# Performance work log

Measured on AMD Instinct MI355X. Metric: run time of the kernel, lower is better.

Reference implementation:

```python
import jax, jax.numpy as jnp
import numpy as np

TEMP = 0.7
EPS = 1e-6
LN_EPS = 1e-5
CAP_FACTOR = 2.0


def setup_inputs() -> dict:
    key = jax.random.key(0)
    B, S, H, E = 8, 4096, 2048, 8
    H2 = H // 2
    ks = jax.random.split(key, 3)
    x = jax.random.normal(ks[0], (B, S, H), jnp.float32)
    ln_w = jnp.ones((H,), jnp.float32)
    ln_b = jnp.zeros((H,), jnp.float32)
    # kaiming_normal_(fan_in, relu): std = sqrt(2 / fan_in)
    w1 = jax.random.normal(ks[1], (H2, H), jnp.float32) * np.float32(np.sqrt(2.0 / H))
    b1 = jnp.zeros((H2,), jnp.float32)
    w2 = jax.random.normal(ks[2], (E, H2), jnp.float32) * np.float32(np.sqrt(2.0 / H2))
    b2 = jnp.zeros((E,), jnp.float32)
    return {"x": x, "ln_w": ln_w, "ln_b": ln_b, "w1": w1, "b1": b1,
            "w2": w2, "b2": b2, "top_k": 2, "num_experts": E}


def _forward(x, ln_w, ln_b, w1, b1, w2, b2, top_k, num_experts):
    B, S, H = x.shape
    N = B * S
    # router: LayerNorm -> Linear -> GELU(exact) -> Linear
    mu = x.mean(-1, keepdims=True)
    var = jnp.mean((x - mu) ** 2, axis=-1, keepdims=True)
    h = (x - mu) * jax.lax.rsqrt(var + LN_EPS) * ln_w + ln_b
    h = jax.nn.gelu(h @ w1.T + b1, approximate=False)
    logits = h @ w2.T + b2
    ew = jnp.clip(logits / TEMP, -50.0, 50.0)  # [B,S,E]

    flat = ew.reshape(N, num_experts)
    capacity = int(CAP_FACTOR * N * top_k / num_experts)

    # top-k per token + softmax over the k selected logits, scatter into dense mask
    tk_w, tk_i = jax.lax.top_k(flat, top_k)          # [N,k]
    sm = jax.nn.softmax(tk_w, axis=-1)               # [N,k]
    rows = jnp.arange(N)[:, None]
    masks = jnp.zeros((N, num_experts), flat.dtype).at[rows, tk_i].set(sm)

    # capacity drop: per expert column, if sum of weights > capacity keep only
    # the top-`capacity` weighted tokens (extra zero-valued picks are no-ops,
    # matching the torch min(capacity, nnz) behavior).
    cols = masks.T                                   # [E,N]
    sums = cols.sum(-1)                              # [E]
    kcap = min(capacity, N)
    tv, ti = jax.lax.top_k(cols, kcap)               # [E,kcap]
    erow = jnp.arange(num_experts)[:, None]
    capped = jnp.zeros_like(cols).at[erow, ti].set(tv)
    over = sums > capacity
    cols = jnp.where(over[:, None], capped, cols)
    count = jax.lax.stop_gradient(jnp.where(over, capped.sum(-1), sums))  # buffer, no grad

    masks = cols.T
    masks = masks / jnp.maximum(masks.sum(-1, keepdims=True), EPS)

    usage = count / jnp.maximum(count.sum(), EPS)
    target = jnp.full((num_experts,), 1.0 / num_experts, usage.dtype)
    # F.kl_div(log(usage), target, reduction='batchmean') with batch dim = E
    kl = jnp.sum(target * (jnp.log(target) - jnp.log(jnp.maximum(usage, EPS)))) / num_experts
    loss = 0.01 * kl
    return ew, masks.reshape(B, S, num_experts), loss, usage


def reference(x, ln_w, ln_b, w1, b1, w2, b2, top_k, num_experts):
    return _forward(x, ln_w, ln_b, w1, b1, w2, b2, top_k, num_experts)
```

## Files before the change

### kernel.cpp

```cpp
#include <hip/hip_runtime.h>
#include <math.h>

#define NTOK 32768
#define HDIM 2048
#define H2DIM 1024
#define NE 8

#define WS_MU 0
#define WS_RS 32768
#define WS_LOGITS 65536
#define WS_SUMS (65536 + 262144)
#define WS_W1_BYTES 1310976ull
#define WS_NEED (WS_W1_BYTES + 8388608ull)

#define OUT_MASKS 262144
#define OUT_LOSS 524288
#define OUT_USAGE 524289

typedef _Float16 half8 __attribute__((ext_vector_type(8)));
typedef float floatx16 __attribute__((ext_vector_type(16)));

#define H_SCALE 0.03125f
#define X_SCALE (0.03125f / 4096.0f)

__global__ __launch_bounds__(256) void w1prep_kernel(const float* __restrict__ w1,
                                                     _Float16* __restrict__ w1p) {
  int idx = blockIdx.x * 256 + threadIdx.x;
  int n = idx >> 6, kc = idx & 63;
  const float4* src = (const float4*)(w1 + (size_t)n * HDIM + kc * 32);
  float wv[32];
#pragma unroll
  for (int v = 0; v < 8; ++v) {
    float4 f = src[v];
    wv[v * 4 + 0] = f.x; wv[v * 4 + 1] = f.y;
    wv[v * 4 + 2] = f.z; wv[v * 4 + 3] = f.w;
  }
  _Float16 hi[32], lo[32];
#pragma unroll
  for (int v = 0; v < 32; ++v) {
    float t = wv[v] * 32.0f;
    hi[v] = (_Float16)t;
    lo[v] = (_Float16)((t - (float)hi[v]) * 4096.0f);
  }
  _Float16* dst = w1p + (size_t)idx * 64;
#pragma unroll
  for (int c = 0; c < 4; ++c) {
    half8 h = {hi[c*8+0],hi[c*8+1],hi[c*8+2],hi[c*8+3],hi[c*8+4],hi[c*8+5],hi[c*8+6],hi[c*8+7]};
    half8 l = {lo[c*8+0],lo[c*8+1],lo[c*8+2],lo[c*8+3],lo[c*8+4],lo[c*8+5],lo[c*8+6],lo[c*8+7]};
    *(half8*)&dst[c * 8] = h;
    *(half8*)&dst[32 + c * 8] = l;
  }
}

__global__ __launch_bounds__(256) void ln_stats_kernel(const float* __restrict__ x,
                                                       float* __restrict__ ws) {
  int g = blockIdx.x * 256 + threadIdx.x;
  if (g < NTOK * NE + NE) ws[WS_LOGITS + g] = 0.0f;

  int row = blockIdx.x * 4 + (threadIdx.x >> 6);
  int lane = threadIdx.x & 63;
  const float4* p = (const float4*)(x + (size_t)row * HDIM);
  float s = 0.f, sq = 0.f;
#pragma unroll
  for (int i = 0; i < 8; ++i) {
    float4 v = p[lane + 64 * i];
    s += (v.x + v.y) + (v.z + v.w);
    sq += (v.x * v.x + v.y * v.y) + (v.z * v.z + v.w * v.w);
  }
#pragma unroll
  for (int o = 32; o > 0; o >>= 1) {
    s += __shfl_xor(s, o);
    sq += __shfl_xor(sq, o);
  }
  if (lane == 0) {
    float m = s * (1.0f / HDIM);
    float var = fmaxf(sq * (1.0f / HDIM) - m * m, 0.0f);
    ws[WS_MU + row] = m;
    ws[WS_RS + row] = 1.0f / sqrtf(var + 1e-5f);
  }
}

#define LDB 40

__global__ __launch_bounds__(256, 2) void gemm_mfma_kernel(
    const float* __restrict__ x, const float* __restrict__ ln_w,
    const float* __restrict__ ln_b, const _Float16* __restrict__ w1p,
    const float* __restrict__ bias1, const float* __restrict__ w2,
    const float* __restrict__ mu, const float* __restrict__ rs,
    float* __restrict__ logits) {
  __shared__ _Float16 Ah[128 * LDB];
  __shared__ _Float16 Al[128 * LDB];
  __shared__ _Float16 Bh[128 * LDB];
  __shared__ _Float16 Bl[128 * LDB];

  const int tid = threadIdx.x;
  const int lin = blockIdx.x;
  const int xcd = lin & 7;
  const int jj = lin >> 3;
  const int m0 = (xcd * 32 + (jj >> 3)) * 128;
  const int n0 = (jj & 7) * 128;

  const int lane = tid & 63;
  const int wid = tid >> 6;
  const int wm = wid >> 1, wn = wid & 1;
  const int fr = lane & 31, fq = lane >> 5;

  const int am = tid >> 1, ak = (tid & 1) * 16;
  const float* xrow = x + (size_t)(m0 + am) * HDIM;
  const float ars = rs[m0 + am];
  const float amrs = -mu[m0 + am] * ars;
  const int bn = tid >> 1, bp = tid & 1;
  const _Float16* bsrc0 = w1p + (size_t)(n0 + bn) * 4096 + bp * 32;
  _Float16* bdst = (bp ? Bl : Bh) + bn * LDB;

  floatx16 acc_hh[2][2], acc_x[2][2];
#pragma unroll
  for (int i = 0; i < 2; ++i)
#pragma unroll
    for (int j = 0; j < 2; ++j)
#pragma unroll
      for (int r = 0; r < 16; ++r) { acc_hh[i][j][r] = 0.f; acc_x[i][j][r] = 0.f; }

  for (int kc = 0; kc < 64; ++kc) {
    const int k0 = kc * 32;
    const float4* xp = (const float4*)(xrow + k0 + ak);
    float4 xv0 = xp[0], xv1 = xp[1], xv2 = xp[2], xv3 = xp[3];
    const float4* lwp = (const float4*)(ln_w + k0 + ak);
    float4 lw0 = lwp[0], lw1 = lwp[1], lw2 = lwp[2], lw3 = lwp[3];
    const float4* lbp = (const float4*)(ln_b + k0 + ak);
    float4 lb0 = lbp[0], lb1 = lbp[1], lb2 = lbp[2], lb3 = lbp[3];
    const float4* bs = (const float4*)(bsrc0 + (size_t)kc * 64);
    float4 bv0 = bs[0], bv1 = bs[1], bv2 = bs[2], bv3 = bs[3];

    float xa[16] = {xv0.x,xv0.y,xv0.z,xv0.w, xv1.x,xv1.y,xv1.z,xv1.w,
                    xv2.x,xv2.y,xv2.z,xv2.w, xv3.x,xv3.y,xv3.z,xv3.w};
    float lwa[16] = {lw0.x,lw0.y,lw0.z,lw0.w, lw1.x,lw1.y,lw1.z,lw1.w,
                     lw2.x,lw2.y,lw2.z,lw2.w, lw3.x,lw3.y,lw3.z,lw3.w};
    float lba[16] = {lb0.x,lb0.y,lb0.z,lb0.w, lb1.x,lb1.y,lb1.z,lb1.w,
                     lb2.x,lb2.y,lb2.z,lb2.w, lb3.x,lb3.y,lb3.z,lb3.w};
    _Float16 hi[16], lo[16];
#pragma unroll
    for (int v = 0; v < 16; ++v) {
      float y = fmaf(fmaf(xa[v], ars, amrs), lwa[v], lba[v]);
      hi[v] = (_Float16)y;
      lo[v] = (_Float16)((y - (float)hi[v]) * 4096.0f);
    }

    __syncthreads();
    {
      half8 h0 = {hi[0],hi[1],hi[2],hi[3],hi[4],hi[5],hi[6],hi[7]};
      half8 h1 = {hi[8],hi[9],hi[10],hi[11],hi[12],hi[13],hi[14],hi[15]};
      half8 l0 = {lo[0],lo[1],lo[2],lo[3],lo[4],lo[5],lo[6],lo[7]};
      half8 l1 = {lo[8],lo[9],lo[10],lo[11],lo[12],lo[13],lo[14],lo[15]};
      *(half8*)&Ah[am * LDB + ak] = h0;
      *(half8*)&Ah[am * LDB + ak + 8] = h1;
      *(half8*)&Al[am * LDB + ak] = l0;
      *(half8*)&Al[am * LDB + ak + 8] = l1;
      float4* bd = (float4*)bdst;
      bd[0] = bv0; bd[1] = bv1; bd[2] = bv2; bd[3] = bv3;
    }
    __syncthreads();

#pragma unroll
    for (int t = 0; t < 2; ++t) {
      half8 ah[2], al[2], bh[2], bl[2];
#pragma unroll
      for (int i = 0; i < 2; ++i) {
        int off = (wm * 64 + i * 32 + fr) * LDB + t * 16 + fq * 8;
        ah[i] = *(const half8*)&Ah[off];
        al[i] = *(const half8*)&Al[off];
      }
#pragma unroll
      for (int j = 0; j < 2; ++j) {
        int off = (wn * 64 + j * 32 + fr) * LDB + t * 16 + fq * 8;
        bh[j] = *(const half8*)&Bh[off];
        bl[j] = *(const half8*)&Bl[off];
      }
#pragma unroll
      for (int i = 0; i < 2; ++i)
#pragma unroll
        for (int j = 0; j < 2; ++j) {
          acc_hh[i][j] = __builtin_amdgcn_mfma_f32_32x32x16_f16(ah[i], bh[j], acc_hh[i][j], 0, 0, 0);
          acc_x[i][j]  = __builtin_amdgcn_mfma_f32_32x32x16_f16(ah[i], bl[j], acc_x[i][j], 0, 0, 0);
          acc_x[i][j]  = __builtin_amdgcn_mfma_f32_32x32x16_f16(al[i], bh[j], acc_x[i][j], 0, 0, 0);
        }
    }
  }

  const float inv_sqrt2 = 0.70710678118654752440f;
  const int c = fr;
  const int col0 = n0 + wn * 64 + c;
  const int col1 = col0 + 32;
  float w2r0[NE], w2r1[NE];
#pragma unroll
  for (int e = 0; e < NE; ++e) {
    w2r0[e] = w2[e * H2DIM + col0];
    w2r1[e] = w2[e * H2DIM + col1];
  }
  const float b10 = bias1[col0], b11 = bias1[col1];

#pragma unroll
  for (int i = 0; i < 2; ++i)
#pragma unroll
    for (int r = 0; r < 16; ++r) {
      int row = m0 + wm * 64 + i * 32 + (r & 3) + 8 * (r >> 2) + 4 * fq;
      float h0 = acc_hh[i][0][r] * H_SCALE + acc_x[i][0][r] * X_SCALE + b10;
      float h1 = acc_hh[i][1][r] * H_SCALE + acc_x[i][1][r] * X_SCALE + b11;
      float g0 = 0.5f * h0 * (1.0f + erff(h0 * inv_sqrt2));
      float g1 = 0.5f * h1 * (1.0f + erff(h1 * inv_sqrt2));
      float pl[NE];
#pragma unroll
      for (int e = 0; e < NE; ++e) pl[e] = fmaf(g0, w2r0[e], g1 * w2r1[e]);
#pragma unroll
      for (int o = 1; o <= 16; o <<= 1)
#pragma unroll
        for (int e = 0; e < NE; ++e) pl[e] += __shfl_xor(pl[e], o);
      if (c == 0) {
#pragma unroll
        for (int e = 0; e < NE; ++e)
          atomicAdd(&logits[(size_t)row * NE + e], pl[e]);
      }
    }
}

#define BM 128
#define BN 128
#define BK 16
#define LDT 132

__global__ __launch_bounds__(256, 2) void gemm1_kernel(
    const float* __restrict__ x, const float* __restrict__ ln_w,
    const float* __restrict__ ln_b, const float* __restrict__ w1,
    const float* __restrict__ bias1, const float* __restrict__ w2,
    const float* __restrict__ mu, const float* __restrict__ rs,
    float* __restrict__ logits) {
  __shared__ float As[BK * LDT];
  __shared__ float Bs[BK * LDT];
  __shared__ float w2s[NE * BN];

  const int tid = threadIdx.x;
  const int n0 = blockIdx.x * BN;
  const int m0 = blockIdx.y * BM;

  for (int i = tid; i < NE * BN; i += 256)
    w2s[i] = w2[(size_t)(i >> 7) * H2DIM + n0 + (i & 127)];

  const int lm0 = tid >> 2;
  const int lm1 = lm0 + 64;
  const int kq = (tid & 3) * 4;
  const float* xa0 = x + (size_t)(m0 + lm0) * HDIM + kq;
  const float* xa1 = x + (size_t)(m0 + lm1) * HDIM + kq;
  const float* wb0 = w1 + (size_t)(n0 + lm0) * HDIM + kq;
  const float* wb1 = w1 + (size_t)(n0 + lm1) * HDIM + kq;
  const float mu0 = mu[m0 + lm0], rs0 = rs[m0 + lm0];
  const float mu1 = mu[m0 + lm1], rs1 = rs[m0 + lm1];

  const int tm = tid >> 4;
  const int tn = tid & 15;

  float acc[8][8] = {};

  for (int k0 = 0; k0 < HDIM; k0 += BK) {
    float4 a0 = *(const float4*)(xa0 + k0);
    float4 a1 = *(const float4*)(xa1 + k0);
    float4 b0 = *(const float4*)(wb0 + k0);
    float4 b1 = *(const float4*)(wb1 + k0);
    float4 lw = *(const float4*)(ln_w + k0 + kq);
    float4 lb = *(const float4*)(ln_b + k0 + kq);
    a0.x = (a0.x - mu0) * rs0 * lw.x + lb.x;
    a0.y = (a0.y - mu0) * rs0 * lw.y + lb.y;
    a0.z = (a0.z - mu0) * rs0 * lw.z + lb.z;
    a0.w = (a0.w - mu0) * rs0 * lw.w + lb.w;
    a1.x = (a1.x - mu1) * rs1 * lw.x + lb.x;
    a1.y = (a1.y - mu1) * rs1 * lw.y + lb.y;
    a1.z = (a1.z - mu1) * rs1 * lw.z + lb.z;
    a1.w = (a1.w - mu1) * rs1 * lw.w + lb.w;
    __syncthreads();
    As[(kq + 0) * LDT + lm0] = a0.x;
    As[(kq + 1) * LDT + lm0] = a0.y;
    As[(kq + 2) * LDT + lm0] = a0.z;
    As[(kq + 3) * LDT + lm0] = a0.w;
    As[(kq + 0) * LDT + lm1] = a1.x;
    As[(kq + 1) * LDT + lm1] = a1.y;
    As[(kq + 2) * LDT + lm1] = a1.z;
    As[(kq + 3) * LDT + lm1] = a1.w;
    Bs[(kq + 0) * LDT + lm0] = b0.x;
    Bs[(kq + 1) * LDT + lm0] = b0.y;
    Bs[(kq + 2) * LDT + lm0] = b0.z;
    Bs[(kq + 3) * LDT + lm0] = b0.w;
    Bs[(kq + 0) * LDT + lm1] = b1.x;
    Bs[(kq + 1) * LDT + lm1] = b1.y;
    Bs[(kq + 2) * LDT + lm1] = b1.z;
    Bs[(kq + 3) * LDT + lm1] = b1.w;
    __syncthreads();
#pragma unroll
    for (int kk = 0; kk < BK; ++kk) {
      float4 aLo = *(const float4*)&As[kk * LDT + tm * 8];
      float4 aHi = *(const float4*)&As[kk * LDT + tm * 8 + 4];
      float4 bLo = *(const float4*)&Bs[kk * LDT + tn * 8];
      float4 bHi = *(const float4*)&Bs[kk * LDT + tn * 8 + 4];
      float av[8] = {aLo.x, aLo.y, aLo.z, aLo.w, aHi.x, aHi.y, aHi.z, aHi.w};
      float bv[8] = {bLo.x, bLo.y, bLo.z, bLo.w, bHi.x, bHi.y, bHi.z, bHi.w};
#pragma unroll
      for (int i = 0; i < 8; ++i)
#pragma unroll
        for (int j = 0; j < 8; ++j) acc[i][j] = fmaf(av[i], bv[j], acc[i][j]);
    }
  }

  const float inv_sqrt2 = 0.70710678118654752440f;
  float bb[8];
#pragma unroll
  for (int j = 0; j < 8; ++j) bb[j] = bias1[n0 + tn * 8 + j];

#pragma unroll
  for (int i = 0; i < 8; ++i) {
    float g[8];
#pragma unroll
    for (int j = 0; j < 8; ++j) {
      float v = acc[i][j] + bb[j];
      g[j] = 0.5f * v * (1.0f + erff(v * inv_sqrt2));
    }
    float pl[NE];
#pragma unroll
    for (int e = 0; e < NE; ++e) {
      float s = 0.f;
#pragma unroll
      for (int j = 0; j < 8; ++j) s = fmaf(g[j], w2s[e * BN + tn * 8 + j], s);
      pl[e] = s;
    }
#pragma unroll
    for (int o = 1; o <= 8; o <<= 1)
#pragma unroll
      for (int e = 0; e < NE; ++e) pl[e] += __shfl_xor(pl[e], o);
    if (tn == 0) {
      int r = m0 + tm * 8 + i;
#pragma unroll
      for (int e = 0; e < NE; ++e)
        atomicAdd(&logits[(size_t)r * NE + e], pl[e]);
    }
  }
}

__global__ __launch_bounds__(256) void route_kernel(const float* __restrict__ logits,
                                                    const float* __restrict__ b2,
                                                    float* __restrict__ out,
                                                    float* __restrict__ sums) {
  __shared__ float ssum[NE];
  if (threadIdx.x < NE) ssum[threadIdx.x] = 0.f;
  __syncthreads();

  int tok = blockIdx.x * 256 + threadIdx.x;
  const float4* lp = (const float4*)(logits + (size_t)tok * NE);
  float4 l0 = lp[0], l1 = lp[1];
  float lv[NE] = {l0.x, l0.y, l0.z, l0.w, l1.x, l1.y, l1.z, l1.w};
  float ew[NE];
#pragma unroll
  for (int e = 0; e < NE; ++e) {
    float v = (lv[e] + b2[e]) / 0.7f;
    ew[e] = fminf(fmaxf(v, -50.0f), 50.0f);
  }

  int i1 = 0;
  float v1 = ew[0];
#pragma unroll
  for (int e = 1; e < NE; ++e)
    if (ew[e] > v1) { v1 = ew[e]; i1 = e; }
  int i2 = -1;
  float v2 = -1e30f;
#pragma unroll
  for (int e = 0; e < NE; ++e)
    if (e != i1 && ew[e] > v2) { v2 = ew[e]; i2 = e; }

  float t = expf(v2 - v1);
  float sm1 = 1.0f / (1.0f + t);
  float sm2 = t / (1.0f + t);
  float rsum = fmaxf(sm1 + sm2, 1e-6f);
  float m1 = sm1 / rsum, m2 = sm2 / rsum;

  float4* oew = (float4*)(out + (size_t)tok * NE);
  oew[0] = make_float4(ew[0], ew[1], ew[2], ew[3]);
  oew[1] = make_float4(ew[4], ew[5], ew[6], ew[7]);

  float mv[NE];
#pragma unroll
  for (int e = 0; e < NE; ++e)
    mv[e] = (e == i1) ? m1 : ((e == i2) ? m2 : 0.0f);
  float4* om = (float4*)(out + OUT_MASKS + (size_t)tok * NE);
  om[0] = make_float4(mv[0], mv[1], mv[2], mv[3]);
  om[1] = make_float4(mv[4], mv[5], mv[6], mv[7]);

  atomicAdd(&ssum[i1], sm1);
  atomicAdd(&ssum[i2], sm2);
  __syncthreads();
  if (threadIdx.x < NE) atomicAdd(&sums[threadIdx.x], ssum[threadIdx.x]);
}

__global__ void finalize_kernel(const float* __restrict__ sums,
                                float* __restrict__ out) {
  if (threadIdx.x != 0 || blockIdx.x != 0) return;
  float c[NE], tot = 0.f;
  for (int e = 0; e < NE; ++e) {
    c[e] = sums[e];
    tot += c[e];
  }
  float target = 1.0f / NE;
  float lt = logf(target);
  float kl = 0.f;
  for (int e = 0; e < NE; ++e) {
    float u = c[e] / fmaxf(tot, 1e-6f);
    out[OUT_USAGE + e] = u;
    kl += target * (lt - logf(fmaxf(u, 1e-6f)));
  }
  out[OUT_LOSS] = 0.01f * (kl / NE);
}

extern "C" void kernel_launch(void* const* d_in, const int* in_sizes, int n_in,
                              void* d_out, int out_size, void* d_ws, size_t ws_size,
                              hipStream_t stream) {
  const float* x = (const float*)d_in[0];
  const float* ln_w = (const float*)d_in[1];
  const float* ln_b = (const float*)d_in[2];
  const float* w1 = (const float*)d_in[3];
  const float* b1 = (const float*)d_in[4];
  const float* w2 = (const float*)d_in[5];
  const float* b2 = (const float*)d_in[6];
  float* out = (float*)d_out;
  float* ws = (float*)d_ws;
  _Float16* w1p = (_Float16*)((char*)d_ws + WS_W1_BYTES);

  const bool use_mfma = ws_size >= WS_NEED;

  ln_stats_kernel<<<NTOK / 4, 256, 0, stream>>>(x, ws);
  if (use_mfma) {
    w1prep_kernel<<<256, 256, 0, stream>>>(w1, w1p);
    gemm_mfma_kernel<<<2048, 256, 0, stream>>>(
        x, ln_w, ln_b, w1p, b1, w2, ws + WS_MU, ws + WS_RS, ws + WS_LOGITS);
  } else {
    gemm1_kernel<<<dim3(H2DIM / BN, NTOK / BM), 256, 0, stream>>>(
        x, ln_w, ln_b, w1, b1, w2, ws + WS_MU, ws + WS_RS, ws + WS_LOGITS);
  }
  route_kernel<<<NTOK / 256, 256, 0, stream>>>(ws + WS_LOGITS, b2, out,
                                               ws + WS_SUMS);
  finalize_kernel<<<1, 64, 0, stream>>>(ws + WS_SUMS, out);
}
```

Before: 1.239 ms.

## Fold LayerNorm into GEMM weights and epilogue, prefetch next K tile

Folds the LayerNorm affine transform into the W1 prep: the weights are pre-multiplied by ln_w, and per-column constants C1 (sum of w·ln_w) and C2 (sum of w·ln_b) are accumulated with atomics. The GEMM then consumes raw x split into hi/lo halves, and mean/rstd are applied per row in the epilogue. This removes the ln_w/ln_b loads and the per-element normalisation FMAs from the main loop. The change also register-prefetches the next x and W tiles, raises occupancy to 3 blocks per SM, and accumulates the cross terms into a temporary that is scaled and added each step. The risks are precision loss, since raw x and the mean-subtraction cancellation can amplify fp16 split error, plus extra register pressure from the prefetch.

```diff
diff --git a/kernel.cpp b/kernel.cpp
--- a/kernel.cpp
+++ b/kernel.cpp
@@ -10,7 +10,9 @@
 #define WS_RS 32768
 #define WS_LOGITS 65536
 #define WS_SUMS (65536 + 262144)
-#define WS_W1_BYTES 1310976ull
+#define WS_C1 (WS_SUMS + NE)
+#define WS_C2 (WS_C1 + 1024)
+#define WS_W1_BYTES 1318976ull
 #define WS_NEED (WS_W1_BYTES + 8388608ull)
 
 #define OUT_MASKS 262144
@@ -21,24 +23,32 @@
 typedef float floatx16 __attribute__((ext_vector_type(16)));
 
 #define H_SCALE 0.03125f
-#define X_SCALE (0.03125f / 4096.0f)
-
-__global__ __launch_bounds__(256) void w1prep_kernel(const float* __restrict__ w1,
-                                                     _Float16* __restrict__ w1p) {
+
+__global__ __launch_bounds__(256) void w1prep_kernel(
+    const float* __restrict__ w1, const float* __restrict__ ln_w,
+    const float* __restrict__ ln_b, _Float16* __restrict__ w1p,
+    float* __restrict__ C1, float* __restrict__ C2) {
   int idx = blockIdx.x * 256 + threadIdx.x;
   int n = idx >> 6, kc = idx & 63;
   const float4* src = (const float4*)(w1 + (size_t)n * HDIM + kc * 32);
-  float wv[32];
+  const float4* lwp = (const float4*)(ln_w + kc * 32);
+  const float4* lbp = (const float4*)(ln_b + kc * 32);
+  float wv[32], lwv[32], lbv[32];
 #pragma unroll
   for (int v = 0; v < 8; ++v) {
-    float4 f = src[v];
-    wv[v * 4 + 0] = f.x; wv[v * 4 + 1] = f.y;
-    wv[v * 4 + 2] = f.z; wv[v * 4 + 3] = f.w;
-  }
+    float4 f = src[v], g = lwp[v], h = lbp[v];
+    wv[v*4+0]=f.x; wv[v*4+1]=f.y; wv[v*4+2]=f.z; wv[v*4+3]=f.w;
+    lwv[v*4+0]=g.x; lwv[v*4+1]=g.y; lwv[v*4+2]=g.z; lwv[v*4+3]=g.w;
+    lbv[v*4+0]=h.x; lbv[v*4+1]=h.y; lbv[v*4+2]=h.z; lbv[v*4+3]=h.w;
+  }
+  float c1 = 0.f, c2 = 0.f;
   _Float16 hi[32], lo[32];
 #pragma unroll
   for (int v = 0; v < 32; ++v) {
-    float t = wv[v] * 32.0f;
+    float wp = wv[v] * lwv[v];
+    c1 += wp;
+    c2 += lbv[v] * wv[v];
+    float t = wp * 32.0f;
     hi[v] = (_Float16)t;
     lo[v] = (_Float16)((t - (float)hi[v]) * 4096.0f);
   }
@@ -50,12 +60,14 @@
     *(half8*)&dst[c * 8] = h;
     *(half8*)&dst[32 + c * 8] = l;
   }
+  atomicAdd(&C1[n], c1);
+  atomicAdd(&C2[n], c2);
 }
 
 __global__ __launch_bounds__(256) void ln_stats_kernel(const float* __restrict__ x,
                                                        float* __restrict__ ws) {
   int g = blockIdx.x * 256 + threadIdx.x;
-  if (g < NTOK * NE + NE) ws[WS_LOGITS + g] = 0.0f;
+  if (g < NTOK * NE + NE + 2048) ws[WS_LOGITS + g] = 0.0f;
 
   int row = blockIdx.x * 4 + (threadIdx.x >> 6);
   int lane = threadIdx.x & 63;
@@ -82,11 +94,11 @@
 
 #define LDB 40
 
-__global__ __launch_bounds__(256, 2) void gemm_mfma_kernel(
-    const float* __restrict__ x, const float* __restrict__ ln_w,
-    const float* __restrict__ ln_b, const _Float16* __restrict__ w1p,
+__global__ __launch_bounds__(256, 3) void gemm_mfma_kernel(
+    const float* __restrict__ x, const _Float16* __restrict__ w1p,
     const float* __restrict__ bias1, const float* __restrict__ w2,
     const float* __restrict__ mu, const float* __restrict__ rs,
+    const float* __restrict__ C1, const float* __restrict__ C2,
     float* __restrict__ logits) {
   __shared__ _Float16 Ah[128 * LDB];
   __shared__ _Float16 Al[128 * LDB];
@@ -106,44 +118,40 @@
   const int fr = lane & 31, fq = lane >> 5;
 
   const int am = tid >> 1, ak = (tid & 1) * 16;
-  const float* xrow = x + (size_t)(m0 + am) * HDIM;
-  const float ars = rs[m0 + am];
-  const float amrs = -mu[m0 + am] * ars;
+  const float* xrow = x + (size_t)(m0 + am) * HDIM + ak;
   const int bn = tid >> 1, bp = tid & 1;
-  const _Float16* bsrc0 = w1p + (size_t)(n0 + bn) * 4096 + bp * 32;
+  const _Float16* bsrc = w1p + (size_t)(n0 + bn) * 4096 + bp * 32;
   _Float16* bdst = (bp ? Bl : Bh) + bn * LDB;
-
-  floatx16 acc_hh[2][2], acc_x[2][2];
+  _Float16* adst_h = Ah + am * LDB + ak;
+  _Float16* adst_l = Al + am * LDB + ak;
+
+  floatx16 acc[2][2];
 #pragma unroll
   for (int i = 0; i < 2; ++i)
 #pragma unroll
     for (int j = 0; j < 2; ++j)
 #pragma unroll
-      for (int r = 0; r < 16; ++r) { acc_hh[i][j][r] = 0.f; acc_x[i][j][r] = 0.f; }
+      for (int r = 0; r < 16; ++r) acc[i][j][r] = 0.f;
+  floatx16 zv;
+#pragma unroll
+  for (int r = 0; r < 16; ++r) zv[r] = 0.f;
+
+  float4 xr0, xr1, xr2, xr3, br0, br1, br2, br3;
+  {
+    const float4* xp = (const float4*)xrow;
+    xr0 = xp[0]; xr1 = xp[1]; xr2 = xp[2]; xr3 = xp[3];
+    const float4* bq = (const float4*)bsrc;
+    br0 = bq[0]; br1 = bq[1]; br2 = bq[2]; br3 = bq[3];
+  }
 
   for (int kc = 0; kc < 64; ++kc) {
-    const int k0 = kc * 32;
-    const float4* xp = (const float4*)(xrow + k0 + ak);
-    float4 xv0 = xp[0], xv1 = xp[1], xv2 = xp[2], xv3 = xp[3];
-    const float4* lwp = (const float4*)(ln_w + k0 + ak);
-    float4 lw0 = lwp[0], lw1 = lwp[1], lw2 = lwp[2], lw3 = lwp[3];
-    const float4* lbp = (const float4*)(ln_b + k0 + ak);
-    float4 lb0 = lbp[0], lb1 = lbp[1], lb2 = lbp[2], lb3 = lbp[3];
-    const float4* bs = (const float4*)(bsrc0 + (size_t)kc * 64);
-    float4 bv0 = bs[0], bv1 = bs[1], bv2 = bs[2], bv3 = bs[3];
-
-    float xa[16] = {xv0.x,xv0.y,xv0.z,xv0.w, xv1.x,xv1.y,xv1.z,xv1.w,
-                    xv2.x,xv2.y,xv2.z,xv2.w, xv3.x,xv3.y,xv3.z,xv3.w};
-    float lwa[16] = {lw0.x,lw0.y,lw0.z,lw0.w, lw1.x,lw1.y,lw1.z,lw1.w,
-                     lw2.x,lw2.y,lw2.z,lw2.w, lw3.x,lw3.y,lw3.z,lw3.w};
-    float lba[16] = {lb0.x,lb0.y,lb0.z,lb0.w, lb1.x,lb1.y,lb1.z,lb1.w,
-                     lb2.x,lb2.y,lb2.z,lb2.w, lb3.x,lb3.y,lb3.z,lb3.w};
+    float xa[16] = {xr0.x,xr0.y,xr0.z,xr0.w, xr1.x,xr1.y,xr1.z,xr1.w,
+                    xr2.x,xr2.y,xr2.z,xr2.w, xr3.x,xr3.y,xr3.z,xr3.w};
     _Float16 hi[16], lo[16];
 #pragma unroll
     for (int v = 0; v < 16; ++v) {
-      float y = fmaf(fmaf(xa[v], ars, amrs), lwa[v], lba[v]);
-      hi[v] = (_Float16)y;
-      lo[v] = (_Float16)((y - (float)hi[v]) * 4096.0f);
+      hi[v] = (_Float16)xa[v];
+      lo[v] = (_Float16)((xa[v] - (float)hi[v]) * 4096.0f);
     }
 
     __syncthreads();
@@ -152,14 +160,21 @@
       half8 h1 = {hi[8],hi[9],hi[10],hi[11],hi[12],hi[13],hi[14],hi[15]};
       half8 l0 = {lo[0],lo[1],lo[2],lo[3],lo[4],lo[5],lo[6],lo[7]};
       half8 l1 = {lo[8],lo[9],lo[10],lo[11],lo[12],lo[13],lo[14],lo[15]};
-      *(half8*)&Ah[am * LDB + ak] = h0;
-      *(half8*)&Ah[am * LDB + ak + 8] = h1;
-      *(half8*)&Al[am * LDB + ak] = l0;
-      *(half8*)&Al[am * LDB + ak + 8] = l1;
+      *(half8*)adst_h = h0;
+      *(half8*)(adst_h + 8) = h1;
+      *(half8*)adst_l = l0;
+      *(half8*)(adst_l + 8) = l1;
       float4* bd = (float4*)bdst;
-      bd[0] = bv0; bd[1] = bv1; bd[2] = bv2; bd[3] = bv3;
+      bd[0] = br0; bd[1] = br1; bd[2] = br2; bd[3] = br3;
     }
     __syncthreads();
+
+    if (kc < 63) {
+      const float4* xp = (const float4*)(xrow + (kc + 1) * 32);
+      xr0 = xp[0]; xr1 = xp[1]; xr2 = xp[2]; xr3 = xp[3];
+      const float4* bq = (const float4*)(bsrc + (size_t)(kc + 1) * 64);
+      br0 = bq[0]; br1 = bq[1]; br2 = bq[2]; br3 = bq[3];
+    }
 
 #pragma unroll
     for (int t = 0; t < 2; ++t) {
@@ -180,9 +195,10 @@
       for (int i = 0; i < 2; ++i)
 #pragma unroll
         for (int j = 0; j < 2; ++j) {
-          acc_hh[i][j] = __builtin_amdgcn_mfma_f32_32x32x16_f16(ah[i], bh[j], acc_hh[i][j], 0, 0, 0);
-          acc_x[i][j]  = __builtin_amdgcn_mfma_f32_32x32x16_f16(ah[i], bl[j], acc_x[i][j], 0, 0, 0);
-          acc_x[i][j]  = __builtin_amdgcn_mfma_f32_32x32x16_f16(al[i], bh[j], acc_x[i][j], 0, 0, 0);
+          acc[i][j] = __builtin_amdgcn_mfma_f32_32x32x16_f16(ah[i], bh[j], acc[i][j], 0, 0, 0);
+          floatx16 tmp = __builtin_amdgcn_mfma_f32_32x32x16_f16(ah[i], bl[j], zv, 0, 0, 0);
+          tmp = __builtin_amdgcn_mfma_f32_32x32x16_f16(al[i], bh[j], tmp, 0, 0, 0);
+          acc[i][j] += tmp * (1.0f / 4096.0f);
         }
     }
   }
@@ -197,15 +213,19 @@
     w2r0[e] = w2[e * H2DIM + col0];
     w2r1[e] = w2[e * H2DIM + col1];
   }
-  const float b10 = bias1[col0], b11 = bias1[col1];
+  const float c1a = C1[col0], c1b = C1[col1];
+  const float hb0 = C2[col0] + bias1[col0];
+  const float hb1 = C2[col1] + bias1[col1];
 
 #pragma unroll
   for (int i = 0; i < 2; ++i)
 #pragma unroll
     for (int r = 0; r < 16; ++r) {
       int row = m0 + wm * 64 + i * 32 + (r & 3) + 8 * (r >> 2) + 4 * fq;
-      float h0 = acc_hh[i][0][r] * H_SCALE + acc_x[i][0][r] * X_SCALE + b10;
-      float h1 = acc_hh[i][1][r] * H_SCALE + acc_x[i][1][r] * X_SCALE + b11;
+      float rsr = rs[row];
+      float nmr = -rsr * mu[row];
+      float h0 = fmaf(acc[i][0][r] * H_SCALE, rsr, fmaf(nmr, c1a, hb0));
+      float h1 = fmaf(acc[i][1][r] * H_SCALE, rsr, fmaf(nmr, c1b, hb1));
       float g0 = 0.5f * h0 * (1.0f + erff(h0 * inv_sqrt2));
       float g1 = 0.5f * h1 * (1.0f + erff(h1 * inv_sqrt2));
       float pl[NE];
@@ -433,9 +453,11 @@
 
   ln_stats_kernel<<<NTOK / 4, 256, 0, stream>>>(x, ws);
   if (use_mfma) {
-    w1prep_kernel<<<256, 256, 0, stream>>>(w1, w1p);
+    w1prep_kernel<<<256, 256, 0, stream>>>(w1, ln_w, ln_b, w1p,
+                                           ws + WS_C1, ws + WS_C2);
     gemm_mfma_kernel<<<2048, 256, 0, stream>>>(
-        x, ln_w, ln_b, w1p, b1, w2, ws + WS_MU, ws + WS_RS, ws + WS_LOGITS);
+        x, w1p, b1, w2, ws + WS_MU, ws + WS_RS, ws + WS_C1, ws + WS_C2,
+        ws + WS_LOGITS);
   } else {
     gemm1_kernel<<<dim3(H2DIM / BN, NTOK / BM), 256, 0, stream>>>(
         x, ln_w, ln_b, w1, b1, w2, ws + WS_MU, ws + WS_RS, ws + WS_LOGITS);
```

Result: faster. 1.177 ms (-5.0%).
